# Performance work log

Measured on AMD Instinct MI355X. Metric: run time of the kernel, lower is better.

## Reference

```python
import jax, jax.numpy as jnp
import numpy as np

S, B, D, H = 1024, 4, 1024, 16
HD = D // H          # 64
MAXREL = 50          # max_relative_position hard-coded in RelativeAttention
EPS = 1e-8


def rmsnorm(x, scale):
    # RMSNorm: x / (||x||_2 / sqrt(d) + eps) * scale
    norm = jnp.sqrt(jnp.sum(x * x, axis=-1, keepdims=True))
    rms = norm * (x.shape[-1] ** -0.5)
    return scale * (x / (rms + EPS))


def rel_embed(table, len_q, len_k):
    # table: [2*MAXREL+1, HD] -> [len_q, len_k, HD]
    dist = jnp.arange(len_k)[None, :] - jnp.arange(len_q)[:, None]
    idx = jnp.clip(dist, -MAXREL, MAXREL) + MAXREL
    return table[idx]


def setup_inputs() -> dict:
    key = jax.random.key(0)
    ks = jax.random.split(key, 16)
    std = 0.02
    inp = {
        'x': jax.random.normal(ks[0], (S, B, D), jnp.float32),
        'Wq': jax.random.normal(ks[1], (D, D), jnp.float32) * std,
        'bq': jnp.zeros((D,), jnp.float32),
        'Wk': jax.random.normal(ks[2], (D, D), jnp.float32) * std,
        'bk': jnp.zeros((D,), jnp.float32),
        'Wv': jax.random.normal(ks[3], (D, D), jnp.float32) * std,
        'bv': jnp.zeros((D,), jnp.float32),
        'Wo': jax.random.normal(ks[4], (D, D), jnp.float32) * std,
        'bo': jnp.zeros((D,), jnp.float32),
        'rel_k': jax.random.normal(ks[5], (2 * MAXREL + 1, HD), jnp.float32) * std,
        'rel_v': jax.random.normal(ks[6], (2 * MAXREL + 1, HD), jnp.float32) * std,
        'g_attn': jnp.ones((D,), jnp.float32),
        'g_ff': jnp.ones((D,), jnp.float32),
        'W_in': jax.random.normal(ks[7], (4 * D, D), jnp.float32) * std,
        'b_in': jnp.zeros((4 * D,), jnp.float32),
        'W_out': jax.random.normal(ks[8], (D, 4 * D), jnp.float32) * std,
        'b_out': jnp.zeros((D,), jnp.float32),
    }
    return inp


def reference(x, Wq, bq, Wk, bk, Wv, bv, Wo, bo, rel_k, rel_v,
              g_attn, g_ff, W_in, b_in, W_out, b_out):
    # --- pre-norm (norm_first=True, rmsnorm) ---
    h = rmsnorm(x, g_attn)                        # [S,B,D]

    # --- RelativeAttention (self-attention, temp_pe=0, no mask) ---
    hb = jnp.transpose(h, (1, 0, 2))              # [B,S,D]
    q = hb @ Wq.T + bq
    k = hb @ Wk.T + bk
    v = hb @ Wv.T + bv
    qh = q.reshape(B, S, H, HD).transpose(0, 2, 1, 3)   # [B,H,S,HD]
    kh = k.reshape(B, S, H, HD).transpose(0, 2, 1, 3)
    vh = v.reshape(B, S, H, HD).transpose(0, 2, 1, 3)

    attn1 = jnp.einsum('bhqd,bhkd->bhqk', qh, kh)
    rk = rel_embed(rel_k, S, S)                          # [q,k,HD]
    attn2 = jnp.einsum('bhqd,qkd->bhqk', qh, rk)
    attn = jax.nn.softmax((attn1 + attn2) / jnp.sqrt(jnp.float32(HD)), axis=-1)

    w1 = jnp.einsum('bhqk,bhkd->bhqd', attn, vh)
    rv = rel_embed(rel_v, S, S)
    w2 = jnp.einsum('bhqk,qkd->bhqd', attn, rv)
    o = (w1 + w2).transpose(0, 2, 1, 3).reshape(B, S, D)
    o = o @ Wo.T + bo
    attn_out = jnp.transpose(o, (1, 0, 2))        # back to [S,B,D]

    # residual onto pre-normed h (faithful to source: h = h + attn)
    h = h + attn_out

    # --- FFN (pre-norm) ---
    ff = rmsnorm(h, g_ff)
    ff = jax.nn.gelu(ff @ W_in.T + b_in, approximate=False)
    ff = ff @ W_out.T + b_out
    return h + ff
```

## Files before the change

### kernel.cpp

```cpp
#include <hip/hip_runtime.h>
#include <hip/hip_bf16.h>

#define S_   1024
#define B_   4
#define D_   1024
#define H_   16
#define HD_  64
#define DFF_ 4096
#define NREL 101
#define MROWS (S_*B_)

typedef __attribute__((ext_vector_type(8))) short bf16x8;
typedef __attribute__((ext_vector_type(4))) float f32x4;

__device__ __forceinline__ float b2f(unsigned short u) {
  unsigned int v = ((unsigned int)u) << 16;
  return __builtin_bit_cast(float, v);
}
__device__ __forceinline__ unsigned short f2b(float f) {
  unsigned int v = __builtin_bit_cast(unsigned int, f);
  v += 0x7fffu + ((v >> 16) & 1u);
  return (unsigned short)(v >> 16);
}

__device__ __forceinline__ float wave_red_sum(float v) {
#pragma unroll
  for (int o = 32; o; o >>= 1) v += __shfl_xor(v, o, 64);
  return v;
}

__device__ __forceinline__ void gload_lds16(const void* g, void* l) {
  __builtin_amdgcn_global_load_lds(
      (const __attribute__((address_space(1))) void*)g,
      (__attribute__((address_space(3))) void*)l, 16, 0, 0);
}

__device__ __forceinline__ void cvt4(const float* s, unsigned short* d, int idx) {
  float4 v = *(const float4*)(s + idx);
  ushort4 o; o.x = f2b(v.x); o.y = f2b(v.y); o.z = f2b(v.z); o.w = f2b(v.w);
  *(ushort4*)(d + idx) = o;
}
__global__ __launch_bounds__(256) void cvt_all(
    const float* __restrict__ Wq, const float* __restrict__ Wk, const float* __restrict__ Wv,
    const float* __restrict__ Wo, const float* __restrict__ W_in, const float* __restrict__ W_out,
    const float* __restrict__ relk,
    unsigned short* __restrict__ wqkvB, unsigned short* __restrict__ woB,
    unsigned short* __restrict__ winB, unsigned short* __restrict__ woutB,
    unsigned short* __restrict__ relkB) {
  int i = (blockIdx.x * 256 + threadIdx.x) * 4;
  const int M1 = 1048576;
  if (i < M1) { cvt4(Wq, wqkvB, i); return; }
  i -= M1;
  if (i < M1) { cvt4(Wk, wqkvB + M1, i); return; }
  i -= M1;
  if (i < M1) { cvt4(Wv, wqkvB + 2 * M1, i); return; }
  i -= M1;
  if (i < M1) { cvt4(Wo, woB, i); return; }
  i -= M1;
  if (i < 4 * M1) { cvt4(W_in, winB, i); return; }
  i -= 4 * M1;
  if (i < 4 * M1) { cvt4(W_out, woutB, i); return; }
  i -= 4 * M1;
  if (i < 7168) {
    if (i < 6464) cvt4(relk, relkB, i);
    else { ushort4 z = {0, 0, 0, 0}; *(ushort4*)(relkB + i) = z; }
  }
}

template<bool TO_BSD, bool WF32>
__global__ __launch_bounds__(256) void rmsnorm_kernel(
    const float* __restrict__ x, const float* __restrict__ g,
    unsigned short* __restrict__ yb, float* __restrict__ yf) {
  const int row = blockIdx.x;
  int orow = row;
  if (TO_BSD) { int s = row >> 2, b = row & 3; orow = b * S_ + s; }
  const float4 v = *(const float4*)(x + (size_t)row * D_ + threadIdx.x * 4);
  float ss = v.x * v.x + v.y * v.y + v.z * v.z + v.w * v.w;
  ss = wave_red_sum(ss);
  __shared__ float red[4];
  if ((threadIdx.x & 63) == 0) red[threadIdx.x >> 6] = ss;
  __syncthreads();
  const float tot = red[0] + red[1] + red[2] + red[3];
  const float inv = 1.f / (sqrtf(tot) * (1.f / 32.f) + 1e-8f);
  const float4 gg = *(const float4*)(g + threadIdx.x * 4);
  const float o0 = gg.x * v.x * inv, o1 = gg.y * v.y * inv;
  const float o2 = gg.z * v.z * inv, o3 = gg.w * v.w * inv;
  const size_t ob = (size_t)orow * D_ + threadIdx.x * 4;
  ushort4 ub; ub.x = f2b(o0); ub.y = f2b(o1); ub.z = f2b(o2); ub.w = f2b(o3);
  *(ushort4*)(yb + ob) = ub;
  if (WF32) { float4 of = make_float4(o0, o1, o2, o3); *(float4*)(yf + ob) = of; }
}

template<int MODE>
__global__ __launch_bounds__(256) void gemm_bf16(
    const unsigned short* __restrict__ X, const unsigned short* __restrict__ Wt,
    const float* __restrict__ bias, const float* __restrict__ resid,
    void* __restrict__ Yv, void* __restrict__ Yv2, void* __restrict__ Yv3,
    int N, int K, int kbeg, int kend) {
  __shared__ __align__(16) unsigned short As[128 * 32];
  __shared__ __align__(16) unsigned short Bs[128 * 32];
  const int tid = threadIdx.x;
  const int wid = tid >> 6, lane = tid & 63;
  const int bm = blockIdx.x * 128, bn = blockIdx.y * 128;
  const int wr = wid >> 1, wc = wid & 1;

  const int klen = kend - kbeg;
  const int kb = kbeg + blockIdx.z * klen;
  const int ke = kb + klen;

  f32x4 acc[4][4];
#pragma unroll
  for (int m = 0; m < 4; ++m)
#pragma unroll
    for (int n = 0; n < 4; ++n) acc[m][n] = (f32x4){0.f, 0.f, 0.f, 0.f};

  const int r0 = wid * 2, r1 = wid * 2 + 1;
  const int sr0 = r0 * 16 + (lane >> 2), sr1 = r1 * 16 + (lane >> 2);
  const int seg = (lane & 3) * 8;
  const int fr = lane & 15, kg = lane >> 4;

  for (int k0 = kb; k0 < ke; k0 += 32) {
    __syncthreads();
    gload_lds16(X + (size_t)(bm + sr0) * K + k0 + seg, As + r0 * 512);
    gload_lds16(X + (size_t)(bm + sr1) * K + k0 + seg, As + r1 * 512);
    gload_lds16(Wt + (size_t)(bn + sr0) * K + k0 + seg, Bs + r0 * 512);
    gload_lds16(Wt + (size_t)(bn + sr1) * K + k0 + seg, Bs + r1 * 512);
    __syncthreads();
    bf16x8 a[4], b[4];
#pragma unroll
    for (int m = 0; m < 4; ++m)
      a[m] = *(const bf16x8*)&As[(wr * 64 + m * 16 + fr) * 32 + kg * 8];
#pragma unroll
    for (int n = 0; n < 4; ++n)
      b[n] = *(const bf16x8*)&Bs[(wc * 64 + n * 16 + fr) * 32 + kg * 8];
    __builtin_amdgcn_s_setprio(1);
#pragma unroll
    for (int m = 0; m < 4; ++m)
#pragma unroll
      for (int n = 0; n < 4; ++n)
        acc[m][n] = __builtin_amdgcn_mfma_f32_16x16x32_bf16(a[m], b[n], acc[m][n], 0, 0, 0);
    __builtin_amdgcn_s_setprio(0);
  }

  const int fq = lane >> 4;
#pragma unroll
  for (int m = 0; m < 4; ++m) {
    const int gr0 = bm + wr * 64 + m * 16 + fq * 4;
#pragma unroll
    for (int n = 0; n < 4; ++n) {
      const int gc = bn + wc * 64 + n * 16 + fr;
      if constexpr (MODE == 5) {
        const int sg = gc >> 10, col = gc & 1023;
        const float bv = bias[gc];
        if (sg == 2) {
          ushort4 st;
          st.x = f2b(acc[m][n][0] + bv); st.y = f2b(acc[m][n][1] + bv);
          st.z = f2b(acc[m][n][2] + bv); st.w = f2b(acc[m][n][3] + bv);
          const int bb = gr0 >> 10, s = gr0 & (S_ - 1);
          *(ushort4*)((unsigned short*)Yv3 + ((size_t)(bb * 1024 + col)) * 1024 + s) = st;
        } else {
          unsigned short* tgt = sg ? (unsigned short*)Yv2 : (unsigned short*)Yv;
#pragma unroll
          for (int r = 0; r < 4; ++r)
            tgt[(size_t)(gr0 + r) * 1024 + col] = f2b(acc[m][n][r] + bv);
        }
      } else if constexpr (MODE == 6) {
        float* pz = blockIdx.z ? (float*)Yv2 : (float*)Yv;
#pragma unroll
        for (int r = 0; r < 4; ++r)
          pz[(size_t)(gr0 + r) * N + gc] = acc[m][n][r];
      } else {
        const float bv = bias[gc];
#pragma unroll
        for (int r = 0; r < 4; ++r) {
          const int row = gr0 + r;
          float v = acc[m][n][r] + bv;
          if constexpr (MODE == 1) {
            ((float*)Yv)[(size_t)row * N + gc] = v + resid[(size_t)row * N + gc];
          } else if constexpr (MODE == 2) {
            v = 0.5f * v * (1.f + erff(v * 0.70710678118654752f));
            ((unsigned short*)Yv)[(size_t)row * N + gc] = f2b(v);
          } else {
            v += resid[(size_t)row * N + gc];
            const int bb = row >> 10, s = row & (S_ - 1);
            ((float*)Yv)[((size_t)(s * B_ + bb)) * D_ + gc] = v;
          }
        }
      }
    }
  }
}

__global__ __launch_bounds__(256) void combine_kernel(
    const float* __restrict__ p0, const float* __restrict__ p1,
    const float* __restrict__ bias, const float* __restrict__ resid,
    float* __restrict__ out) {
  const int row = blockIdx.x;
  const int col = threadIdx.x * 4;
  const size_t idx = (size_t)row * D_ + col;
  float4 a = *(const float4*)(p0 + idx);
  float4 b = *(const float4*)(p1 + idx);
  float4 r = *(const float4*)(resid + idx);
  float4 bb = *(const float4*)(bias + col);
  float4 v = make_float4(a.x + b.x + r.x + bb.x, a.y + b.y + r.y + bb.y,
                         a.z + b.z + r.z + bb.z, a.w + b.w + r.w + bb.w);
  const int bbi = row >> 10, s = row & (S_ - 1);
  *(float4*)(out + ((size_t)(s * B_ + bbi)) * D_ + col) = v;
}

__global__ __launch_bounds__(256, 4) void attn_mfma(
    const unsigned short* __restrict__ Q, const unsigned short* __restrict__ Kb,
    const unsigned short* __restrict__ vT, const unsigned short* __restrict__ relkB,
    const float* __restrict__ relv, unsigned short* __restrict__ Wctx) {
  __shared__ unsigned short Pb[16 * 1024];
  __shared__ float qrelp[16 * 112];
  __shared__ float redmx[16 * 4];
  __shared__ float redsm[16 * 4];
  __shared__ float prp[2 * 16 * 4];

  const int q0 = blockIdx.x * 16;
  const int bh = blockIdx.y, b = bh >> 4, h = bh & 15;
  const int tid = threadIdx.x, w = tid >> 6, lane = tid & 63;
  const int fr = lane & 15, kg = lane >> 4;
  const size_t base = ((size_t)b * S_) * D_ + h * HD_;

  bf16x8 qa0 = *(const bf16x8*)(Q + base + (size_t)(q0 + fr) * D_ + kg * 8);
  bf16x8 qa1 = *(const bf16x8*)(Q + base + (size_t)(q0 + fr) * D_ + 32 + kg * 8);

  for (int rt = w; rt < 7; rt += 4) {
    f32x4 c = (f32x4){0.f, 0.f, 0.f, 0.f};
    bf16x8 b0 = *(const bf16x8*)(relkB + (rt * 16 + fr) * 64 + kg * 8);
    bf16x8 b1 = *(const bf16x8*)(relkB + (rt * 16 + fr) * 64 + 32 + kg * 8);
    c = __builtin_amdgcn_mfma_f32_16x16x32_bf16(qa0, b0, c, 0, 0, 0);
    c = __builtin_amdgcn_mfma_f32_16x16x32_bf16(qa1, b1, c, 0, 0, 0);
#pragma unroll
    for (int rr = 0; rr < 4; ++rr)
      qrelp[(kg * 4 + rr) * 112 + rt * 16 + fr] = c[rr];
  }
  __syncthreads();

  const int kbase = w * 16 + fr;
  f32x4 c[16];
#pragma unroll
  for (int j = 0; j < 16; ++j) {
    const unsigned short* kp = Kb + base + (size_t)(j * 64 + kbase) * D_ + kg * 8;
    bf16x8 kf0 = *(const bf16x8*)(kp);
    bf16x8 kf1 = *(const bf16x8*)(kp + 32);
    f32x4 t = (f32x4){0.f, 0.f, 0.f, 0.f};
    t = __builtin_amdgcn_mfma_f32_16x16x32_bf16(qa0, kf0, t, 0, 0, 0);
    t = __builtin_amdgcn_mfma_f32_16x16x32_bf16(qa1, kf1, t, 0, 0, 0);
    c[j] = t;
  }
#pragma unroll
  for (int j = 0; j < 16; ++j) {
    const int k = j * 64 + kbase;
#pragma unroll
    for (int rr = 0; rr < 4; ++rr) {
      const int q = kg * 4 + rr;
      const int ridx = min(max(k - (q0 + q), -50), 50) + 50;
      c[j][rr] = (c[j][rr] + qrelp[q * 112 + ridx]) * 0.125f;
    }
  }

  float mx[4];
#pragma unroll
  for (int rr = 0; rr < 4; ++rr) {
    float m = c[0][rr];
#pragma unroll
    for (int j = 1; j < 16; ++j) m = fmaxf(m, c[j][rr]);
#pragma unroll
    for (int o = 1; o <= 8; o <<= 1) m = fmaxf(m, __shfl_xor(m, o, 64));
    mx[rr] = m;
  }
  if (fr == 0) {
#pragma unroll
    for (int rr = 0; rr < 4; ++rr) redmx[(kg * 4 + rr) * 4 + w] = mx[rr];
  }
  __syncthreads();
  float m[4];
#pragma unroll
  for (int rr = 0; rr < 4; ++rr) {
    const int q = kg * 4 + rr;
    m[rr] = fmaxf(fmaxf(redmx[q * 4 + 0], redmx[q * 4 + 1]),
                  fmaxf(redmx[q * 4 + 2], redmx[q * 4 + 3]));
  }

#pragma unroll
  for (int j = 0; j < 16; ++j)
#pragma unroll
    for (int rr = 0; rr < 4; ++rr) c[j][rr] = __expf(c[j][rr] - m[rr]);

  float sm[4], sl[4], sr4[4];
#pragma unroll
  for (int rr = 0; rr < 4; ++rr) { sm[rr] = 0.f; sl[rr] = 0.f; sr4[rr] = 0.f; }
#pragma unroll
  for (int j = 0; j < 16; ++j) {
    const int k = j * 64 + kbase;
#pragma unroll
    for (int rr = 0; rr < 4; ++rr) {
      const int d = k - (q0 + kg * 4 + rr);
      const float e = c[j][rr];
      sm[rr] += e;
      sl[rr] += (d <= -50) ? e : 0.f;
      sr4[rr] += (d >= 50) ? e : 0.f;
    }
  }
#pragma unroll
  for (int rr = 0; rr < 4; ++rr) {
#pragma unroll
    for (int o = 1; o <= 8; o <<= 1) {
      sm[rr] += __shfl_xor(sm[rr], o, 64);
      sl[rr] += __shfl_xor(sl[rr], o, 64);
      sr4[rr] += __shfl_xor(sr4[rr], o, 64);
    }
  }
  if (fr == 0) {
#pragma unroll
    for (int rr = 0; rr < 4; ++rr) {
      const int q = kg * 4 + rr;
      redsm[q * 4 + w] = sm[rr];
      prp[q * 4 + w] = sl[rr];
      prp[64 + q * 4 + w] = sr4[rr];
    }
  }

#pragma unroll
  for (int j = 0; j < 16; ++j) {
    const int k = j * 64 + kbase;
    const int g = k >> 3, kl = k & 7;
#pragma unroll
    for (int rr = 0; rr < 4; ++rr) {
      const int q = kg * 4 + rr;
      const int swb = (q & 7) ^ ((q & 8) >> 2);
      Pb[q * 1024 + ((g ^ swb) << 3) + kl] = f2b(c[j][rr]);
    }
  }
  __syncthreads();

  const int dtile = w * 16;
  const size_t vtb = ((size_t)(b * 1024 + h * 64 + dtile + fr)) * 1024;
  const int swbf = (fr & 7) ^ ((fr & 8) >> 2);
  const unsigned short* pbase = Pb + fr * 1024;
  f32x4 o = (f32x4){0.f, 0.f, 0.f, 0.f};
  __builtin_amdgcn_s_setprio(1);
#pragma unroll 8
  for (int ks = 0; ks < 32; ++ks) {
    bf16x8 va = *(const bf16x8*)(vT + vtb + ks * 32 + kg * 8);
    bf16x8 pb = *(const bf16x8*)(pbase + (((ks * 4 + kg) ^ swbf) << 3));
    o = __builtin_amdgcn_mfma_f32_16x16x32_bf16(va, pb, o, 0, 0, 0);
  }
  __builtin_amdgcn_s_setprio(0);

  const int q = fr;
  const int dl = kg * 4;
  const float rs = redsm[q * 4 + 0] + redsm[q * 4 + 1] +
                   redsm[q * 4 + 2] + redsm[q * 4 + 3];
  const float rinv = 1.f / rs;
  const float slt = prp[q * 4 + 0] + prp[q * 4 + 1] + prp[q * 4 + 2] + prp[q * 4 + 3];
  const float srt = prp[64 + q * 4 + 0] + prp[64 + q * 4 + 1] +
                    prp[64 + q * 4 + 2] + prp[64 + q * 4 + 3];
  f32x4 w2;
  {
    const float4 rv0 = *(const float4*)&relv[0 * 64 + dtile + dl];
    const float4 rv100 = *(const float4*)&relv[100 * 64 + dtile + dl];
    w2[0] = slt * rv0.x + srt * rv100.x;
    w2[1] = slt * rv0.y + srt * rv100.y;
    w2[2] = slt * rv0.z + srt * rv100.z;
    w2[3] = slt * rv0.w + srt * rv100.w;
  }
  const int qi = q0 + q;
  const unsigned short* prow = Pb + q * 1024;
#pragma unroll 4
  for (int r = 1; r < 100; ++r) {
    const int k = qi + r - 50;
    float p = 0.f;
    if (k >= 0 && k < S_)
      p = b2f(prow[(((k >> 3) ^ swbf) << 3) + (k & 7)]);
    const float4 rv = *(const float4*)&relv[r * 64 + dtile + dl];
    w2[0] = fmaf(p, rv.x, w2[0]); w2[1] = fmaf(p, rv.y, w2[1]);
    w2[2] = fmaf(p, rv.z, w2[2]); w2[3] = fmaf(p, rv.w, w2[3]);
  }
  ushort4 st;
  st.x = f2b((o[0] + w2[0]) * rinv);
  st.y = f2b((o[1] + w2[1]) * rinv);
  st.z = f2b((o[2] + w2[2]) * rinv);
  st.w = f2b((o[3] + w2[3]) * rinv);
  *(ushort4*)(Wctx + base + (size_t)qi * D_ + dtile + dl) = st;
}

extern "C" void kernel_launch(void* const* d_in, const int* in_sizes, int n_in,
                              void* d_out, int out_size, void* d_ws, size_t ws_size,
                              hipStream_t stream) {
  (void)in_sizes; (void)n_in; (void)out_size;
  const float* x      = (const float*)d_in[0];
  const float* Wq     = (const float*)d_in[1];
  const float* bq     = (const float*)d_in[2];
  const float* Wk     = (const float*)d_in[3];
  const float* bk     = (const float*)d_in[4];
  const float* Wv     = (const float*)d_in[5];
  const float* bv     = (const float*)d_in[6];
  const float* Wo     = (const float*)d_in[7];
  const float* bo     = (const float*)d_in[8];
  const float* rel_k  = (const float*)d_in[9];
  const float* rel_v  = (const float*)d_in[10];
  const float* g_attn = (const float*)d_in[11];
  const float* g_ff   = (const float*)d_in[12];
  const float* W_in   = (const float*)d_in[13];
  const float* b_in   = (const float*)d_in[14];
  const float* W_out  = (const float*)d_in[15];
  const float* b_out  = (const float*)d_in[16];
  float* out = (float*)d_out;

  const size_t MB = 1u << 20;
  char* Wp = (char*)d_ws;
  float*          hbF  = (float*)Wp;
  unsigned short* hbB  = (unsigned short*)(Wp + 16 * MB);
  unsigned short* qB   = (unsigned short*)(Wp + 24 * MB);
  unsigned short* kB   = (unsigned short*)(Wp + 32 * MB);
  unsigned short* vT   = (unsigned short*)(Wp + 40 * MB);
  unsigned short* wB   = (unsigned short*)(Wp + 48 * MB);
  unsigned short* ff1B = (unsigned short*)(Wp + 24 * MB);
  float*          h2   = (float*)(Wp + 56 * MB);
  unsigned short* fB   = (unsigned short*)(Wp + 72 * MB);
  unsigned short* wqkvB= (unsigned short*)(Wp + 80 * MB);
  unsigned short* woB  = (unsigned short*)(Wp + 86 * MB);
  unsigned short* winB = (unsigned short*)(Wp + 88 * MB);
  unsigned short* woutB= (unsigned short*)(Wp + 96 * MB);
  unsigned short* relkB= (unsigned short*)(Wp + 104 * MB);
  float*          bqkvC= (float*)(Wp + 104 * MB + 16384);
  float*          p0   = hbF;
  float*          p1   = (float*)(Wp + 105 * MB);
  const bool splitK = (ws_size >= 121 * MB);

  hipLaunchKernelGGL(cvt_all, dim3(12295), dim3(256), 0, stream,
                     Wq, Wk, Wv, Wo, W_in, W_out, rel_k,
                     wqkvB, woB, winB, woutB, relkB);
  hipMemcpyAsync(bqkvC,        bq, D_ * sizeof(float), hipMemcpyDeviceToDevice, stream);
  hipMemcpyAsync(bqkvC + D_,   bk, D_ * sizeof(float), hipMemcpyDeviceToDevice, stream);
  hipMemcpyAsync(bqkvC + 2*D_, bv, D_ * sizeof(float), hipMemcpyDeviceToDevice, stream);

  hipLaunchKernelGGL((rmsnorm_kernel<true, true>), dim3(MROWS), dim3(256), 0, stream,
                     x, g_attn, hbB, hbF);
  hipLaunchKernelGGL((gemm_bf16<5>), dim3(MROWS / 128, 3072 / 128), dim3(256), 0, stream,
                     hbB, wqkvB, bqkvC, nullptr, qB, kB, vT, 3072, D_, 0, D_);
  hipLaunchKernelGGL(attn_mfma, dim3(S_ / 16, B_ * H_), dim3(256), 0, stream,
                     qB, kB, vT, relkB, rel_v, wB);
  hipLaunchKernelGGL((gemm_bf16<1>), dim3(MROWS / 128, D_ / 128), dim3(256), 0, stream,
                     wB, woB, bo, hbF, h2, nullptr, nullptr, D_, D_, 0, D_);
  hipLaunchKernelGGL((rmsnorm_kernel<false, false>), dim3(MROWS), dim3(256), 0, stream,
                     h2, g_ff, fB, nullptr);
  hipLaunchKernelGGL((gemm_bf16<2>), dim3(MROWS / 128, DFF_ / 128), dim3(256), 0, stream,
                     fB, winB, b_in, nullptr, ff1B, nullptr, nullptr, DFF_, D_, 0, D_);
  if (splitK) {
    hipLaunchKernelGGL((gemm_bf16<6>), dim3(MROWS / 128, D_ / 128, 2), dim3(256), 0, stream,
                       ff1B, woutB, b_out, nullptr, p0, p1, nullptr, D_, DFF_, 0, DFF_ / 2);
    hipLaunchKernelGGL(combine_kernel, dim3(MROWS), dim3(256), 0, stream,
                       p0, p1, b_out, h2, out);
  } else {
    hipLaunchKernelGGL((gemm_bf16<3>), dim3(MROWS / 128, D_ / 128), dim3(256), 0, stream,
                       ff1B, woutB, b_out, h2, out, nullptr, nullptr, D_, DFF_, 0, DFF_);
  }
}
```

Before: 539.8 us.

## Compute relative-value term with MFMA and remap attention grid for locality

The scalar 99-iteration FMA loop for the relative-value term is replaced by four extra bf16 MFMAs. The band of probabilities, including the clipped-edge sums, is gathered into a padded LDS buffer, and rel_v is pre-transposed to bf16 in the conversion kernel. The attention launch also becomes a 1D grid with a permuted block-to-(batch,head) mapping, which is meant to improve cache locality across concurrently running blocks. The cost is an extra barrier and an LDS staging pass, plus bf16 rounding of rel_v and the edge sums.

```diff
diff --git a/kernel.cpp b/kernel.cpp
--- a/kernel.cpp
+++ b/kernel.cpp
@@ -43,10 +43,10 @@
 __global__ __launch_bounds__(256) void cvt_all(
     const float* __restrict__ Wq, const float* __restrict__ Wk, const float* __restrict__ Wv,
     const float* __restrict__ Wo, const float* __restrict__ W_in, const float* __restrict__ W_out,
-    const float* __restrict__ relk,
+    const float* __restrict__ relk, const float* __restrict__ relv,
     unsigned short* __restrict__ wqkvB, unsigned short* __restrict__ woB,
     unsigned short* __restrict__ winB, unsigned short* __restrict__ woutB,
-    unsigned short* __restrict__ relkB) {
+    unsigned short* __restrict__ relkB, unsigned short* __restrict__ relvT) {
   int i = (blockIdx.x * 256 + threadIdx.x) * 4;
   const int M1 = 1048576;
   if (i < M1) { cvt4(Wq, wqkvB, i); return; }
@@ -64,6 +64,17 @@
   if (i < 7168) {
     if (i < 6464) cvt4(relk, relkB, i);
     else { ushort4 z = {0, 0, 0, 0}; *(ushort4*)(relkB + i) = z; }
+    return;
+  }
+  i -= 7168;
+  if (i < 8192) {
+    const int d = i >> 7, r = i & 127;
+    ushort4 o;
+    o.x = (r     < NREL) ? f2b(relv[(r    ) * 64 + d]) : (unsigned short)0;
+    o.y = (r + 1 < NREL) ? f2b(relv[(r + 1) * 64 + d]) : (unsigned short)0;
+    o.z = (r + 2 < NREL) ? f2b(relv[(r + 2) * 64 + d]) : (unsigned short)0;
+    o.w = (r + 3 < NREL) ? f2b(relv[(r + 3) * 64 + d]) : (unsigned short)0;
+    *(ushort4*)(relvT + i) = o;
   }
 }
 
@@ -211,15 +222,18 @@
 __global__ __launch_bounds__(256, 4) void attn_mfma(
     const unsigned short* __restrict__ Q, const unsigned short* __restrict__ Kb,
     const unsigned short* __restrict__ vT, const unsigned short* __restrict__ relkB,
-    const float* __restrict__ relv, unsigned short* __restrict__ Wctx) {
+    const unsigned short* __restrict__ relvT, unsigned short* __restrict__ Wctx) {
   __shared__ unsigned short Pb[16 * 1024];
   __shared__ float qrelp[16 * 112];
   __shared__ float redmx[16 * 4];
   __shared__ float redsm[16 * 4];
   __shared__ float prp[2 * 16 * 4];
 
-  const int q0 = blockIdx.x * 16;
-  const int bh = blockIdx.y, b = bh >> 4, h = bh & 15;
+  const int id = blockIdx.x;
+  const int low = id & 63;
+  const int bh = (low & 7) * 8 + (low >> 3);
+  const int q0 = (id >> 6) * 16;
+  const int b = bh >> 4, h = bh & 15;
   const int tid = threadIdx.x, w = tid >> 6, lane = tid & 63;
   const int fr = lane & 15, kg = lane >> 4;
   const size_t base = ((size_t)b * S_) * D_ + h * HD_;
@@ -334,6 +348,26 @@
       const int swb = (q & 7) ^ ((q & 8) >> 2);
       Pb[q * 1024 + ((g ^ swb) << 3) + kl] = f2b(c[j][rr]);
     }
+  }
+  __syncthreads();
+
+  unsigned short* prb = (unsigned short*)qrelp;
+  for (int e = tid; e < 16 * 136; e += 256) {
+    const int q = e / 136, r = e - q * 136;
+    unsigned short v = 0;
+    if (r == 0) {
+      v = f2b(prp[q * 4 + 0] + prp[q * 4 + 1] + prp[q * 4 + 2] + prp[q * 4 + 3]);
+    } else if (r == 100) {
+      v = f2b(prp[64 + q * 4 + 0] + prp[64 + q * 4 + 1] +
+              prp[64 + q * 4 + 2] + prp[64 + q * 4 + 3]);
+    } else if (r < 100) {
+      const int k = q0 + q + r - 50;
+      if (k >= 0 && k < S_) {
+        const int swb = (q & 7) ^ ((q & 8) >> 2);
+        v = Pb[q * 1024 + (((k >> 3) ^ swb) << 3) + (k & 7)];
+      }
+    }
+    prb[q * 136 + r] = v;
   }
   __syncthreads();
 
@@ -349,6 +383,12 @@
     bf16x8 pb = *(const bf16x8*)(pbase + (((ks * 4 + kg) ^ swbf) << 3));
     o = __builtin_amdgcn_mfma_f32_16x16x32_bf16(va, pb, o, 0, 0, 0);
   }
+#pragma unroll
+  for (int ks = 0; ks < 4; ++ks) {
+    bf16x8 ra = *(const bf16x8*)(relvT + (dtile + fr) * 128 + ks * 32 + kg * 8);
+    bf16x8 pv = *(const bf16x8*)(prb + fr * 136 + ks * 32 + kg * 8);
+    o = __builtin_amdgcn_mfma_f32_16x16x32_bf16(ra, pv, o, 0, 0, 0);
+  }
   __builtin_amdgcn_s_setprio(0);
 
   const int q = fr;
@@ -356,36 +396,12 @@
   const float rs = redsm[q * 4 + 0] + redsm[q * 4 + 1] +
                    redsm[q * 4 + 2] + redsm[q * 4 + 3];
   const float rinv = 1.f / rs;
-  const float slt = prp[q * 4 + 0] + prp[q * 4 + 1] + prp[q * 4 + 2] + prp[q * 4 + 3];
-  const float srt = prp[64 + q * 4 + 0] + prp[64 + q * 4 + 1] +
-                    prp[64 + q * 4 + 2] + prp[64 + q * 4 + 3];
-  f32x4 w2;
-  {
-    const float4 rv0 = *(const float4*)&relv[0 * 64 + dtile + dl];
-    const float4 rv100 = *(const float4*)&relv[100 * 64 + dtile + dl];
-    w2[0] = slt * rv0.x + srt * rv100.x;
-    w2[1] = slt * rv0.y + srt * rv100.y;
-    w2[2] = slt * rv0.z + srt * rv100.z;
-    w2[3] = slt * rv0.w + srt * rv100.w;
-  }
-  const int qi = q0 + q;
-  const unsigned short* prow = Pb + q * 1024;
-#pragma unroll 4
-  for (int r = 1; r < 100; ++r) {
-    const int k = qi + r - 50;
-    float p = 0.f;
-    if (k >= 0 && k < S_)
-      p = b2f(prow[(((k >> 3) ^ swbf) << 3) + (k & 7)]);
-    const float4 rv = *(const float4*)&relv[r * 64 + dtile + dl];
-    w2[0] = fmaf(p, rv.x, w2[0]); w2[1] = fmaf(p, rv.y, w2[1]);
-    w2[2] = fmaf(p, rv.z, w2[2]); w2[3] = fmaf(p, rv.w, w2[3]);
-  }
   ushort4 st;
-  st.x = f2b((o[0] + w2[0]) * rinv);
-  st.y = f2b((o[1] + w2[1]) * rinv);
-  st.z = f2b((o[2] + w2[2]) * rinv);
-  st.w = f2b((o[3] + w2[3]) * rinv);
-  *(ushort4*)(Wctx + base + (size_t)qi * D_ + dtile + dl) = st;
+  st.x = f2b(o[0] * rinv);
+  st.y = f2b(o[1] * rinv);
+  st.z = f2b(o[2] * rinv);
+  st.w = f2b(o[3] * rinv);
+  *(ushort4*)(Wctx + base + (size_t)(q0 + q) * D_ + dtile + dl) = st;
 }
 
 extern "C" void kernel_launch(void* const* d_in, const int* in_sizes, int n_in,
@@ -428,13 +444,14 @@
   unsigned short* woutB= (unsigned short*)(Wp + 96 * MB);
   unsigned short* relkB= (unsigned short*)(Wp + 104 * MB);
   float*          bqkvC= (float*)(Wp + 104 * MB + 16384);
+  unsigned short* relvT= (unsigned short*)(Wp + 104 * MB + 32768);
   float*          p0   = hbF;
   float*          p1   = (float*)(Wp + 105 * MB);
   const bool splitK = (ws_size >= 121 * MB);
 
-  hipLaunchKernelGGL(cvt_all, dim3(12295), dim3(256), 0, stream,
-                     Wq, Wk, Wv, Wo, W_in, W_out, rel_k,
-                     wqkvB, woB, winB, woutB, relkB);
+  hipLaunchKernelGGL(cvt_all, dim3(12303), dim3(256), 0, stream,
+                     Wq, Wk, Wv, Wo, W_in, W_out, rel_k, rel_v,
+                     wqkvB, woB, winB, woutB, relkB, relvT);
   hipMemcpyAsync(bqkvC,        bq, D_ * sizeof(float), hipMemcpyDeviceToDevice, stream);
   hipMemcpyAsync(bqkvC + D_,   bk, D_ * sizeof(float), hipMemcpyDeviceToDevice, stream);
   hipMemcpyAsync(bqkvC + 2*D_, bv, D_ * sizeof(float), hipMemcpyDeviceToDevice, stream);
@@ -443,8 +460,8 @@
                      x, g_attn, hbB, hbF);
   hipLaunchKernelGGL((gemm_bf16<5>), dim3(MROWS / 128, 3072 / 128), dim3(256), 0, stream,
                      hbB, wqkvB, bqkvC, nullptr, qB, kB, vT, 3072, D_, 0, D_);
-  hipLaunchKernelGGL(attn_mfma, dim3(S_ / 16, B_ * H_), dim3(256), 0, stream,
-                     qB, kB, vT, relkB, rel_v, wB);
+  hipLaunchKernelGGL(attn_mfma, dim3(4096), dim3(256), 0, stream,
+                     qB, kB, vT, relkB, relvT, wB);
   hipLaunchKernelGGL((gemm_bf16<1>), dim3(MROWS / 128, D_ / 128), dim3(256), 0, stream,
                      wB, woB, bo, hbF, h2, nullptr, nullptr, D_, D_, 0, D_);
   hipLaunchKernelGGL((rmsnorm_kernel<false, false>), dim3(MROWS), dim3(256), 0, stream,
```

After: 481.9 us. 1.12x faster.
